# Kernel tuning notes

Hardware: AMD Instinct MI355X
Metric: run time of the kernel (lower is better)

The kernel has to match this reference:

```python
import jax, jax.numpy as jnp
import numpy as np
from jax import lax

KERNEL_SIZE = 2  # init kwarg erode_kernel


def _min_filter_same(x, k):
    """Separable k x k min-filter (erosion) over the last two dims of NCHW x,
    SAME output size, out-of-bounds padded with +inf (matches cv2.erode's
    default border value, which never wins the min)."""
    inf = jnp.asarray(jnp.inf, x.dtype)
    # rows pass then cols pass; square min-filter is separable
    y = lax.reduce_window(x, inf, lax.min,
                          window_dimensions=(1, 1, k, 1),
                          window_strides=(1, 1, 1, 1),
                          padding='SAME')
    y = lax.reduce_window(y, inf, lax.min,
                          window_dimensions=(1, 1, 1, k),
                          window_strides=(1, 1, 1, 1),
                          padding='SAME')
    return y


def setup_inputs() -> dict:
    key = jax.random.key(0)
    x = jax.random.normal(key, (32, 3, 512, 512), dtype=jnp.float32)
    return {"x": x, "l": 1, "gpu": 0}


def reference(x, l, gpu):
    # iterations_times = 4 * (l + 2 - 1); erosion window grows by 2*iters
    iterations_times = 4 * (l + 1)
    k = KERNEL_SIZE + 2 * iterations_times  # 18 for l=1
    # original: tensor2pil(e * 0.5 + 0.5) -> cv2.erode -> pil2tensor ([0,1])
    # (uint8 quantization of the PIL round-trip is omitted; same min-filter math)
    y = x * 0.5 + 0.5
    y = _min_filter_same(y, k)
    return y
```

## Files before the change

kernel.cpp:

```cpp
#include <hip/hip_runtime.h>


#define IMG 512
#define RLO 8

__global__ __launch_bounds__(256, 8)
void erode_fused_22187801051678(const float* __restrict__ in,
                                float* __restrict__ out) {
    __shared__ float B[32][145];

    const int tid = threadIdx.x;
    const int w0 = blockIdx.x * 128;
    const int h0 = blockIdx.y * 32;
    const size_t plane = (size_t)blockIdx.z * (size_t)(IMG * IMG);

    for (int u = tid; u < 290; u += 256) {
        int col, seg;
        if (u < 145) { col = u;       seg = 0; }
        else         { col = u - 145; seg = 1; }
        const int gw  = w0 - RLO + col;
        const bool wok = (unsigned)gw < (unsigned)IMG;
        const int ghb = h0 - RLO + seg * 16;

        float x[33];
#pragma unroll
        for (int i = 0; i < 33; ++i) {
            const int gh = ghb + i;
            float v = __builtin_inff();
            if (wok && (unsigned)gh < (unsigned)IMG)
                v = in[plane + (size_t)gh * IMG + gw];
            x[i] = v;
        }
        float p[32];
#pragma unroll
        for (int i = 0; i < 32; ++i) p[i] = fminf(x[i], x[i + 1]);
        float q[30];
#pragma unroll
        for (int i = 0; i < 30; ++i) q[i] = fminf(p[i], p[i + 2]);
#pragma unroll
        for (int j = 0; j < 16; ++j) {
            float m = fminf(fminf(q[j], q[j + 4]), fminf(q[j + 8], q[j + 12]));
            B[seg * 16 + j][col] = fminf(m, p[j + 16]);
        }
    }
    __syncthreads();

    {
        const int r  = tid & 31;
        const int c8 = tid >> 5;
        float y[33];
#pragma unroll
        for (int i = 0; i < 33; ++i) y[i] = B[r][c8 * 16 + i];
        float p[32];
#pragma unroll
        for (int i = 0; i < 32; ++i) p[i] = fminf(y[i], y[i + 1]);
        float q[30];
#pragma unroll
        for (int i = 0; i < 30; ++i) q[i] = fminf(p[i], p[i + 2]);
        float o[16];
#pragma unroll
        for (int j = 0; j < 16; ++j) {
            float m = fminf(fminf(q[j], q[j + 4]), fminf(q[j + 8], q[j + 12]));
            o[j] = fminf(m, p[j + 16]) * 0.5f + 0.5f;
        }
        float* op = out + plane + (size_t)(h0 + r) * IMG + (w0 + c8 * 16);
#pragma unroll
        for (int jj = 0; jj < 4; ++jj)
            *reinterpret_cast<float4*>(op + 4 * jj) =
                make_float4(o[4 * jj], o[4 * jj + 1], o[4 * jj + 2], o[4 * jj + 3]);
    }
}

extern "C" void kernel_launch(void* const* d_in, const int* in_sizes, int n_in,
                              void* d_out, int out_size, void* d_ws, size_t ws_size,
                              hipStream_t stream) {
    const float* x = (const float*)d_in[0];
    float* out = (float*)d_out;
    const int planes = in_sizes[0] / (IMG * IMG);
    dim3 grid(IMG / 128, IMG / 32, planes);
    erode_fused_22187801051678<<<grid, dim3(256), 0, stream>>>(x, out);
}
```

Before: 194.7 us.

## Use float4 vertical pass, taller tiles, and shared-core horizontal min

The tile height doubles to 64 rows, which shrinks the fraction of halo rows re-read per block. The vertical pass now loads float4 columns and builds the 18-row window minima with shared suffix and prefix minima over 8-row segments. The horizontal pass reads float4 values from shared memory, and each thread makes 4 outputs that share one common core minimum. This cuts global load instruction count and ALU work, at the cost of launch bounds dropping to 4 blocks per SM and more shared memory per block.

```diff
diff --git a/kernel.cpp b/kernel.cpp
--- a/kernel.cpp
+++ b/kernel.cpp
@@ -2,72 +2,88 @@
 
 
 #define IMG 512
-#define RLO 8
 
-__global__ __launch_bounds__(256, 8)
+__device__ __forceinline__ float4 f4min(float4 a, float4 b) {
+    return make_float4(fminf(a.x, b.x), fminf(a.y, b.y),
+                       fminf(a.z, b.z), fminf(a.w, b.w));
+}
+
+__global__ __launch_bounds__(256, 4)
 void erode_fused_22187801051678(const float* __restrict__ in,
                                 float* __restrict__ out) {
-    __shared__ float B[32][145];
+    __shared__ float4 B4[64][38];
 
     const int tid = threadIdx.x;
     const int w0 = blockIdx.x * 128;
-    const int h0 = blockIdx.y * 32;
+    const int h0 = blockIdx.y * 64;
     const size_t plane = (size_t)blockIdx.z * (size_t)(IMG * IMG);
 
-    for (int u = tid; u < 290; u += 256) {
-        int col, seg;
-        if (u < 145) { col = u;       seg = 0; }
-        else         { col = u - 145; seg = 1; }
-        const int gw  = w0 - RLO + col;
-        const bool wok = (unsigned)gw < (unsigned)IMG;
-        const int ghb = h0 - RLO + seg * 16;
+    const float4 VINF = make_float4(__builtin_inff(), __builtin_inff(),
+                                    __builtin_inff(), __builtin_inff());
 
-        float x[33];
+    for (int u = tid; u < 296; u += 256) {
+        const int c = u % 37;
+        const int s = u / 37;
+        const int cb = w0 - 8 + 4 * c;
+        const bool wok = (unsigned)cb < (unsigned)IMG;
+        const int rbase = h0 + 8 * s - 8;
+        const float* bp = in + plane + cb;
+
+#define LD(i) ((wok && (unsigned)(rbase + (i)) < (unsigned)IMG)               \
+                   ? *reinterpret_cast<const float4*>(                        \
+                         bp + (size_t)(rbase + (i)) * IMG)                    \
+                   : VINF)
+
+        float4 S[8];
+        float4 rs = LD(17);
 #pragma unroll
-        for (int i = 0; i < 33; ++i) {
-            const int gh = ghb + i;
-            float v = __builtin_inff();
-            if (wok && (unsigned)gh < (unsigned)IMG)
-                v = in[plane + (size_t)gh * IMG + gw];
-            x[i] = v;
+        for (int i = 16; i >= 0; --i) {
+            rs = f4min(rs, LD(i));
+            if (i < 8) S[i] = rs;
         }
-        float p[32];
+        const int rb = 8 * s;
+        B4[rb + 0][c] = S[0];
+        float4 rp = LD(18);
+        B4[rb + 1][c] = f4min(S[1], rp);
 #pragma unroll
-        for (int i = 0; i < 32; ++i) p[i] = fminf(x[i], x[i + 1]);
-        float q[30];
-#pragma unroll
-        for (int i = 0; i < 30; ++i) q[i] = fminf(p[i], p[i + 2]);
-#pragma unroll
-        for (int j = 0; j < 16; ++j) {
-            float m = fminf(fminf(q[j], q[j + 4]), fminf(q[j + 8], q[j + 12]));
-            B[seg * 16 + j][col] = fminf(m, p[j + 16]);
+        for (int i = 19; i <= 24; ++i) {
+            rp = f4min(rp, LD(i));
+            B4[rb + (i - 17)][c] = f4min(S[i - 17], rp);
         }
+#undef LD
     }
     __syncthreads();
 
-    {
-        const int r  = tid & 31;
-        const int c8 = tid >> 5;
-        float y[33];
+    const int gq = tid & 31;
+    const int r0 = tid >> 5;
 #pragma unroll
-        for (int i = 0; i < 33; ++i) y[i] = B[r][c8 * 16 + i];
-        float p[32];
+    for (int sw = 0; sw < 8; ++sw) {
+        const int r = r0 + 8 * sw;
+        float z[24];
 #pragma unroll
-        for (int i = 0; i < 32; ++i) p[i] = fminf(y[i], y[i + 1]);
-        float q[30];
-#pragma unroll
-        for (int i = 0; i < 30; ++i) q[i] = fminf(p[i], p[i + 2]);
-        float o[16];
-#pragma unroll
-        for (int j = 0; j < 16; ++j) {
-            float m = fminf(fminf(q[j], q[j + 4]), fminf(q[j + 8], q[j + 12]));
-            o[j] = fminf(m, p[j + 16]) * 0.5f + 0.5f;
+        for (int k = 0; k < 6; ++k) {
+            const float4 v = B4[r][gq + k];
+            z[4 * k + 0] = v.x; z[4 * k + 1] = v.y;
+            z[4 * k + 2] = v.z; z[4 * k + 3] = v.w;
         }
-        float* op = out + plane + (size_t)(h0 + r) * IMG + (w0 + c8 * 16);
-#pragma unroll
-        for (int jj = 0; jj < 4; ++jj)
-            *reinterpret_cast<float4*>(op + 4 * jj) =
-                make_float4(o[4 * jj], o[4 * jj + 1], o[4 * jj + 2], o[4 * jj + 3]);
+        const float a0 = fminf(z[3], z[4]);
+        const float a1 = fminf(z[5], z[6]);
+        const float a2 = fminf(z[7], z[8]);
+        const float a3 = fminf(z[9], z[10]);
+        const float a4 = fminf(z[11], z[12]);
+        const float a5 = fminf(z[13], z[14]);
+        const float a6 = fminf(z[15], z[16]);
+        const float b0 = fminf(a0, a1), b1 = fminf(a2, a3);
+        const float b2 = fminf(a4, a5), b3 = fminf(a6, z[17]);
+        const float core = fminf(fminf(b0, b1), fminf(b2, b3));
+        const float o0 = fminf(fminf(z[0], z[1]), fminf(z[2], core));
+        const float o1 = fminf(fminf(z[1], z[2]), fminf(core, z[18]));
+        const float o2 = fminf(fminf(z[2], core), fminf(z[18], z[19]));
+        const float o3 = fminf(fminf(core, z[18]), fminf(z[19], z[20]));
+        const float4 res = make_float4(o0 * 0.5f + 0.5f, o1 * 0.5f + 0.5f,
+                                       o2 * 0.5f + 0.5f, o3 * 0.5f + 0.5f);
+        *reinterpret_cast<float4*>(
+            out + plane + (size_t)(h0 + r) * IMG + (w0 + 4 * gq)) = res;
     }
 }
 
@@ -77,6 +93,6 @@
     const float* x = (const float*)d_in[0];
     float* out = (float*)d_out;
     const int planes = in_sizes[0] / (IMG * IMG);
-    dim3 grid(IMG / 128, IMG / 32, planes);
+    dim3 grid(IMG / 128, IMG / 64, planes);
     erode_fused_22187801051678<<<grid, dim3(256), 0, stream>>>(x, out);
 }
```

New measurement: 202.1 us. 3.8% more time.
